# Optimization experiments

Hardware: AMD Instinct MI355X
Metric: run time of the kernel (lower is better)

Reference implementation:

```python
import jax, jax.numpy as jnp
import numpy as np

P = 7      # pool_size
R = 128    # num_rois
KB = 8     # static max bin extent = floor(wh_max / P) = floor(56/7)


def setup_inputs() -> dict:
    key = jax.random.key(0)
    k1, k2, k3 = jax.random.split(key, 3)
    x = jax.random.normal(k1, (1, 256, 64, 64), dtype=jnp.float32)
    xy = jax.random.randint(k2, (R, 2), 0, 8)            # top-left corners
    wh = jax.random.randint(k3, (R, 2), P, 57)           # w,h in [7,56]: every bin non-empty
    rois = jnp.concatenate([xy, wh], axis=1).astype(jnp.int32)  # [R,4] = (x,y,w,h)
    return {"x": x, "rois": rois}


def _bin_indices(coord, size, limit):
    # Replicates: x1 = int(x + ix*rl); x2 = int(x1 + rl); clamp to [0, limit].
    rl = size.astype(jnp.float32) / P                                    # [R]
    starts = jnp.floor(coord[:, None].astype(jnp.float32)
                       + jnp.arange(P, dtype=jnp.float32) * rl[:, None]).astype(jnp.int32)  # [R,P]
    ends = starts + jnp.floor(rl).astype(jnp.int32)[:, None]             # [R,P]
    starts = jnp.maximum(starts, 0)
    ends = jnp.minimum(ends, limit)
    idx = starts[:, :, None] + jnp.arange(KB, dtype=jnp.int32)           # [R,P,KB]
    valid = idx < ends[:, :, None]
    return jnp.clip(idx, 0, limit - 1), valid


def reference(x, rois):
    B, C, H, W = x.shape
    NEG = jnp.finfo(x.dtype).min
    idx_x, val_x = _bin_indices(rois[:, 0], rois[:, 2], W)   # [R,P,KB]
    idx_y, val_y = _bin_indices(rois[:, 1], rois[:, 3], H)   # [R,P,KB]

    def pool_one(iy, vy, ix, vx):
        # iy,ix: [P,KB] row/col indices for this roi's bins; vy,vx: validity masks
        g = jnp.where(vy[None, None, :, :, None], x[:, :, iy, :], NEG).max(axis=3)  # [B,C,P,W]
        g = jnp.where(vx[None, None, None, :, :], g[:, :, :, ix], NEG).max(axis=4)  # [B,C,Py,Px]
        return g

    out = jax.vmap(pool_one)(idx_y, val_y, idx_x, val_x)     # [R,B,C,P,P]
    # torch: view(-1, num_rois, P, P, C).permute(0,1,4,2,3) -> [1, R, C, P, P] (valid for B=1)
    return out.transpose(1, 0, 2, 3, 4)
```

## Files before the change

kernel.cpp:

```cpp
#include <hip/hip_runtime.h>

#define R 128
#define C 256
#define P 7
#define HW 64
#define SW 72

__global__ __launch_bounds__(256) void
roi_pool_kernel(const float* __restrict__ x,
                const int* __restrict__ rois,
                float* __restrict__ out) {
    const int lane = threadIdx.x & 63;
    const int wid  = __builtin_amdgcn_readfirstlane(threadIdx.x >> 6);
    const int gw   = blockIdx.x * 4 + wid;
    const int c = gw & (C - 1);
    const int r = gw >> 8;

    __shared__ float vmbuf[4][P * SW];
    float* slab = vmbuf[wid];

    const int rx = rois[r * 4 + 0];
    const int ry = rois[r * 4 + 1];
    const int rw = rois[r * 4 + 2];
    const int rh = rois[r * 4 + 3];

    const float rlx = (float)rw / 7.0f;
    const float rly = (float)rh / 7.0f;
    const int kw = __builtin_amdgcn_readfirstlane((int)rlx);
    const int kh = __builtin_amdgcn_readfirstlane((int)rly);

    const int syv = (int)floorf(__fadd_rn((float)ry, __fmul_rn((float)lane, rly)));

    const float* xc = x + (size_t)c * (HW * HW);
    const float NEG = -3.402823466e38f;

#define BAND(PY, KH)                                                         \
    {                                                                        \
        const int sy = __builtin_amdgcn_readlane(syv, PY);                   \
        const float* p = xc + sy * HW + lane;                                \
        float v[KH];                                                         \
        _Pragma("unroll")                                                    \
        for (int j = 0; j < KH; ++j) v[j] = p[j * HW];                       \
        float vm = NEG;                                                      \
        _Pragma("unroll")                                                    \
        for (int j = 0; j < KH; ++j) vm = fmaxf(vm, (j < kh) ? v[j] : NEG);  \
        slab[PY * SW + lane] = vm;                                           \
    }

    if (kh <= 4) {
        BAND(0,4) BAND(1,4) BAND(2,4) BAND(3,4) BAND(4,4) BAND(5,4) BAND(6,4)
    } else {
        BAND(0,8) BAND(1,8) BAND(2,8) BAND(3,8) BAND(4,8) BAND(5,8) BAND(6,8)
    }
#undef BAND

    if (lane < P * P) {
        const int py = lane / 7;
        const int px = lane - py * 7;
        const int sx = (int)floorf(__fadd_rn((float)rx, __fmul_rn((float)px, rlx)));
        const float* wp = slab + py * SW + sx;
        float m = NEG;
        if (kw <= 4) {
            float v0 = wp[0], v1 = wp[1], v2 = wp[2], v3 = wp[3];
            m = v0;
            m = fmaxf(m, (1 < kw) ? v1 : NEG);
            m = fmaxf(m, (2 < kw) ? v2 : NEG);
            m = fmaxf(m, (3 < kw) ? v3 : NEG);
        } else {
            float v0 = wp[0], v1 = wp[1], v2 = wp[2], v3 = wp[3];
            float v4 = wp[4], v5 = wp[5], v6 = wp[6], v7 = wp[7];
            m = fmaxf(fmaxf(fmaxf(v0, v1), fmaxf(v2, v3)), v4);
            m = fmaxf(m, (5 < kw) ? v5 : NEG);
            m = fmaxf(m, (6 < kw) ? v6 : NEG);
            m = fmaxf(m, (7 < kw) ? v7 : NEG);
        }
        out[(size_t)gw * (P * P) + lane] = m;
    }
}

extern "C" void kernel_launch(void* const* d_in, const int* in_sizes, int n_in,
                              void* d_out, int out_size, void* d_ws, size_t ws_size,
                              hipStream_t stream) {
    const float* x = (const float*)d_in[0];
    const int* rois = (const int*)d_in[1];
    float* out = (float*)d_out;

    const int grid = (R * C) / 4;
    roi_pool_kernel<<<grid, 256, 0, stream>>>(x, rois, out);
}
```

Baseline: 17.01 us.

## Process two channels per wavefront and skip loads for columns outside ROI

Each wavefront now handles two adjacent channels, halving the grid and sharing the ROI setup, the readlane row starts and the index math across both channels. Row loads are issued only for lanes whose column lies inside the ROI width, which cuts global memory traffic. Masked-off lanes leave stale shared memory, but the column stage reads only in-ROI columns. The trade-off is fewer waves to hide latency and roughly twice the register and LDS use per wave.

```diff
diff --git a/kernel.cpp b/kernel.cpp
--- a/kernel.cpp
+++ b/kernel.cpp
@@ -13,10 +13,10 @@
     const int lane = threadIdx.x & 63;
     const int wid  = __builtin_amdgcn_readfirstlane(threadIdx.x >> 6);
     const int gw   = blockIdx.x * 4 + wid;
-    const int c = gw & (C - 1);
-    const int r = gw >> 8;
+    const int cp = gw & 127;
+    const int r  = gw >> 7;
 
-    __shared__ float vmbuf[4][P * SW];
+    __shared__ float vmbuf[4][2 * P * SW];
     float* slab = vmbuf[wid];
 
     const int rx = rois[r * 4 + 0];
@@ -30,27 +30,45 @@
     const int kh = __builtin_amdgcn_readfirstlane((int)rly);
 
     const int syv = (int)floorf(__fadd_rn((float)ry, __fmul_rn((float)lane, rly)));
+    const int sy0 = __builtin_amdgcn_readlane(syv, 0);
+    const int sy1 = __builtin_amdgcn_readlane(syv, 1);
+    const int sy2 = __builtin_amdgcn_readlane(syv, 2);
+    const int sy3 = __builtin_amdgcn_readlane(syv, 3);
+    const int sy4 = __builtin_amdgcn_readlane(syv, 4);
+    const int sy5 = __builtin_amdgcn_readlane(syv, 5);
+    const int sy6 = __builtin_amdgcn_readlane(syv, 6);
 
-    const float* xc = x + (size_t)c * (HW * HW);
+    const float* xc0 = x + ((size_t)cp << 13);
     const float NEG = -3.402823466e38f;
+    const bool act = (unsigned)(lane - rx) < (unsigned)rw;
 
-#define BAND(PY, KH)                                                         \
-    {                                                                        \
-        const int sy = __builtin_amdgcn_readlane(syv, PY);                   \
-        const float* p = xc + sy * HW + lane;                                \
-        float v[KH];                                                         \
-        _Pragma("unroll")                                                    \
-        for (int j = 0; j < KH; ++j) v[j] = p[j * HW];                       \
-        float vm = NEG;                                                      \
-        _Pragma("unroll")                                                    \
-        for (int j = 0; j < KH; ++j) vm = fmaxf(vm, (j < kh) ? v[j] : NEG);  \
-        slab[PY * SW + lane] = vm;                                           \
+#define BAND(PY, SY, KH)                                                      \
+    {                                                                         \
+        const float* p = xc0 + (SY) * HW + lane;                              \
+        float v0[KH], v1[KH];                                                 \
+        _Pragma("unroll")                                                     \
+        for (int j = 0; j < KH; ++j) { v0[j] = p[j * HW];                     \
+                                       v1[j] = p[j * HW + 4096]; }            \
+        float m0 = NEG, m1 = NEG;                                             \
+        _Pragma("unroll")                                                     \
+        for (int j = 0; j < KH; ++j) {                                        \
+            m0 = fmaxf(m0, (j < kh) ? v0[j] : NEG);                           \
+            m1 = fmaxf(m1, (j < kh) ? v1[j] : NEG);                           \
+        }                                                                     \
+        slab[(PY) * SW + lane] = m0;                                          \
+        slab[(P + (PY)) * SW + lane] = m1;                                    \
     }
 
     if (kh <= 4) {
-        BAND(0,4) BAND(1,4) BAND(2,4) BAND(3,4) BAND(4,4) BAND(5,4) BAND(6,4)
+        if (act) {
+            BAND(0,sy0,4) BAND(1,sy1,4) BAND(2,sy2,4) BAND(3,sy3,4)
+            BAND(4,sy4,4) BAND(5,sy5,4) BAND(6,sy6,4)
+        }
     } else {
-        BAND(0,8) BAND(1,8) BAND(2,8) BAND(3,8) BAND(4,8) BAND(5,8) BAND(6,8)
+        if (act) {
+            BAND(0,sy0,8) BAND(1,sy1,8) BAND(2,sy2,8) BAND(3,sy3,8)
+            BAND(4,sy4,8) BAND(5,sy5,8) BAND(6,sy6,8)
+        }
     }
 #undef BAND
 
@@ -58,23 +76,30 @@
         const int py = lane / 7;
         const int px = lane - py * 7;
         const int sx = (int)floorf(__fadd_rn((float)rx, __fmul_rn((float)px, rlx)));
-        const float* wp = slab + py * SW + sx;
-        float m = NEG;
+        const float* w0 = slab + py * SW + sx;
+        const float* w1 = w0 + P * SW;
+        float m0, m1;
         if (kw <= 4) {
-            float v0 = wp[0], v1 = wp[1], v2 = wp[2], v3 = wp[3];
-            m = v0;
-            m = fmaxf(m, (1 < kw) ? v1 : NEG);
-            m = fmaxf(m, (2 < kw) ? v2 : NEG);
-            m = fmaxf(m, (3 < kw) ? v3 : NEG);
+            float a0 = w0[0], a1 = w0[1], a2 = w0[2], a3 = w0[3];
+            float b0 = w1[0], b1 = w1[1], b2 = w1[2], b3 = w1[3];
+            m0 = a0; m1 = b0;
+            m0 = fmaxf(m0, (1 < kw) ? a1 : NEG); m1 = fmaxf(m1, (1 < kw) ? b1 : NEG);
+            m0 = fmaxf(m0, (2 < kw) ? a2 : NEG); m1 = fmaxf(m1, (2 < kw) ? b2 : NEG);
+            m0 = fmaxf(m0, (3 < kw) ? a3 : NEG); m1 = fmaxf(m1, (3 < kw) ? b3 : NEG);
         } else {
-            float v0 = wp[0], v1 = wp[1], v2 = wp[2], v3 = wp[3];
-            float v4 = wp[4], v5 = wp[5], v6 = wp[6], v7 = wp[7];
-            m = fmaxf(fmaxf(fmaxf(v0, v1), fmaxf(v2, v3)), v4);
-            m = fmaxf(m, (5 < kw) ? v5 : NEG);
-            m = fmaxf(m, (6 < kw) ? v6 : NEG);
-            m = fmaxf(m, (7 < kw) ? v7 : NEG);
+            float a0 = w0[0], a1 = w0[1], a2 = w0[2], a3 = w0[3];
+            float a4 = w0[4], a5 = w0[5], a6 = w0[6], a7 = w0[7];
+            float b0 = w1[0], b1 = w1[1], b2 = w1[2], b3 = w1[3];
+            float b4 = w1[4], b5 = w1[5], b6 = w1[6], b7 = w1[7];
+            m0 = fmaxf(fmaxf(fmaxf(a0, a1), fmaxf(a2, a3)), a4);
+            m1 = fmaxf(fmaxf(fmaxf(b0, b1), fmaxf(b2, b3)), b4);
+            m0 = fmaxf(m0, (5 < kw) ? a5 : NEG); m1 = fmaxf(m1, (5 < kw) ? b5 : NEG);
+            m0 = fmaxf(m0, (6 < kw) ? a6 : NEG); m1 = fmaxf(m1, (6 < kw) ? b6 : NEG);
+            m0 = fmaxf(m0, (7 < kw) ? a7 : NEG); m1 = fmaxf(m1, (7 < kw) ? b7 : NEG);
         }
-        out[(size_t)gw * (P * P) + lane] = m;
+        const size_t base = ((size_t)(r << 8) + (cp << 1)) * (P * P) + lane;
+        out[base] = m0;
+        out[base + P * P] = m1;
     }
 }
 
@@ -85,6 +110,6 @@
     const int* rois = (const int*)d_in[1];
     float* out = (float*)d_out;
 
-    const int grid = (R * C) / 4;
+    const int grid = (R * C / 2) / 4;
     roi_pool_kernel<<<grid, 256, 0, stream>>>(x, rois, out);
 }
```

Result: slower. 17.67 us (+3.9%).

## Split each (roi, channel) band reduction across two wavefronts with block sync

Applied to the files above, without the earlier changes.

Each (roi, channel) task now uses two wavefronts instead of one. One wave reduces row bands 0-3 and the other reduces bands 4-6 into a shared slab, and a __syncthreads precedes the column reduction done by the first wave. The grid doubles to keep every task covered. This shortens the per-wave serial load chain and adds parallelism, at the cost of a block barrier, an idle second wave during the final phase, and twice as many wavefronts launched.

```diff
diff --git a/kernel.cpp b/kernel.cpp
--- a/kernel.cpp
+++ b/kernel.cpp
@@ -12,12 +12,13 @@
                 float* __restrict__ out) {
     const int lane = threadIdx.x & 63;
     const int wid  = __builtin_amdgcn_readfirstlane(threadIdx.x >> 6);
-    const int gw   = blockIdx.x * 4 + wid;
-    const int c = gw & (C - 1);
-    const int r = gw >> 8;
+    const int half = wid & 1;
+    const int tb   = blockIdx.x * 2 + (wid >> 1);
+    const int c = tb & (C - 1);
+    const int r = tb >> 8;
 
-    __shared__ float vmbuf[4][P * SW];
-    float* slab = vmbuf[wid];
+    __shared__ float vmbuf[2][P * SW];
+    float* slab = vmbuf[wid >> 1];
 
     const int rx = rois[r * 4 + 0];
     const int ry = rois[r * 4 + 1];
@@ -41,40 +42,44 @@
         float v[KH];                                                         \
         _Pragma("unroll")                                                    \
         for (int j = 0; j < KH; ++j) v[j] = p[j * HW];                       \
-        float vm = NEG;                                                      \
+        float vm = v[0];                                        \
         _Pragma("unroll")                                                    \
-        for (int j = 0; j < KH; ++j) vm = fmaxf(vm, (j < kh) ? v[j] : NEG);  \
-        slab[PY * SW + lane] = vm;                                           \
+        for (int j = 1; j < KH; ++j) vm = fmaxf(vm, (j < kh) ? v[j] : NEG);  \
+        slab[(PY) * SW + lane] = vm;                                         \
     }
 
-    if (kh <= 4) {
-        BAND(0,4) BAND(1,4) BAND(2,4) BAND(3,4) BAND(4,4) BAND(5,4) BAND(6,4)
+    if (half == 0) {
+        if (kh <= 4) { BAND(0,4) BAND(1,4) BAND(2,4) BAND(3,4) }
+        else         { BAND(0,8) BAND(1,8) BAND(2,8) BAND(3,8) }
     } else {
-        BAND(0,8) BAND(1,8) BAND(2,8) BAND(3,8) BAND(4,8) BAND(5,8) BAND(6,8)
+        if (kh <= 4) { BAND(4,4) BAND(5,4) BAND(6,4) }
+        else         { BAND(4,8) BAND(5,8) BAND(6,8) }
     }
 #undef BAND
 
-    if (lane < P * P) {
+    __syncthreads();
+
+    if (half == 0 && lane < P * P) {
         const int py = lane / 7;
         const int px = lane - py * 7;
         const int sx = (int)floorf(__fadd_rn((float)rx, __fmul_rn((float)px, rlx)));
-        const float* wp = slab + py * SW + sx;
-        float m = NEG;
+        const float* w = slab + py * SW + sx;
+        float m;
         if (kw <= 4) {
-            float v0 = wp[0], v1 = wp[1], v2 = wp[2], v3 = wp[3];
-            m = v0;
-            m = fmaxf(m, (1 < kw) ? v1 : NEG);
-            m = fmaxf(m, (2 < kw) ? v2 : NEG);
-            m = fmaxf(m, (3 < kw) ? v3 : NEG);
+            float a0 = w[0], a1 = w[1], a2 = w[2], a3 = w[3];
+            m = a0;
+            m = fmaxf(m, (1 < kw) ? a1 : NEG);
+            m = fmaxf(m, (2 < kw) ? a2 : NEG);
+            m = fmaxf(m, (3 < kw) ? a3 : NEG);
         } else {
-            float v0 = wp[0], v1 = wp[1], v2 = wp[2], v3 = wp[3];
-            float v4 = wp[4], v5 = wp[5], v6 = wp[6], v7 = wp[7];
-            m = fmaxf(fmaxf(fmaxf(v0, v1), fmaxf(v2, v3)), v4);
-            m = fmaxf(m, (5 < kw) ? v5 : NEG);
-            m = fmaxf(m, (6 < kw) ? v6 : NEG);
-            m = fmaxf(m, (7 < kw) ? v7 : NEG);
+            float a0 = w[0], a1 = w[1], a2 = w[2], a3 = w[3];
+            float a4 = w[4], a5 = w[5], a6 = w[6], a7 = w[7];
+            m = fmaxf(fmaxf(fmaxf(a0, a1), fmaxf(a2, a3)), a4);
+            m = fmaxf(m, (5 < kw) ? a5 : NEG);
+            m = fmaxf(m, (6 < kw) ? a6 : NEG);
+            m = fmaxf(m, (7 < kw) ? a7 : NEG);
         }
-        out[(size_t)gw * (P * P) + lane] = m;
+        out[(size_t)tb * (P * P) + lane] = m;
     }
 }
 
@@ -85,6 +90,6 @@
     const int* rois = (const int*)d_in[1];
     float* out = (float*)d_out;
 
-    const int grid = (R * C) / 4;
+    const int grid = R * C / 2;
     roi_pool_kernel<<<grid, 256, 0, stream>>>(x, rois, out);
 }
```

New measurement: 17.46 us. +2.7%, slower.
